# Optimization experiments

Hardware: AMD Instinct MI355X
Metric: run time of the kernel (lower is better)

Reference implementation:

```python
import jax, jax.numpy as jnp
import numpy as np

B, T, DIM, H = 32, 1024, 512, 8
HD = DIM // H
HID = int(DIM * 4.0)
EPS = 1e-6
SCALE = HD ** -0.5


def _ln(t, g, b):
    m = t.mean(-1, keepdims=True)
    var = ((t - m) ** 2).mean(-1, keepdims=True)
    return (t - m) * jax.lax.rsqrt(var + EPS) * g + b


def setup_inputs() -> dict:
    key = jax.random.key(0)
    ks = jax.random.split(key, 10)
    n = lambda k, s: jax.random.normal(k, s, dtype=jnp.float32)
    w = lambda k, s: n(k, s) * 0.02
    z = lambda d: jnp.zeros((d,), dtype=jnp.float32)
    o = lambda d: jnp.ones((d,), dtype=jnp.float32)
    return {
        'x': n(ks[0], (B, T, DIM)),
        'k': n(ks[1], (T, H, B, HD)),
        'v': n(ks[2], (T, H, B, HD)),
        'Wqkv': w(ks[3], (DIM, 3 * DIM)), 'bqkv': z(3 * DIM),
        'Wsa': w(ks[4], (DIM, DIM)), 'bsa': z(DIM),
        'Wq': w(ks[5], (DIM, DIM)), 'bq': z(DIM),
        'Wed': w(ks[6], (DIM, DIM)), 'bed': z(DIM),
        'g1': o(DIM), 'be1': z(DIM),
        'g2': o(DIM), 'be2': z(DIM),
        'g3': o(DIM), 'be3': z(DIM),
        'W1': w(ks[7], (DIM, HID)), 'b1': z(HID),
        'W2': w(ks[8], (HID, DIM)), 'b2': z(DIM),
    }


def _decoder_block(x, k, v, Wqkv, bqkv, Wsa, bsa, Wq, bq, Wed, bed,
                   g1, be1, g2, be2, g3, be3, W1, b1, W2, b2):
    # ---- self-attention (faithful to the original, degenerate einsums) ----
    qkv = x @ Wqkv + bqkv                                        # [B,T,3*DIM]
    qkv = qkv.reshape(B, T, 3, H, HD).transpose(2, 1, 3, 0, 4)   # [3,T,H,B,HD]
    q, sk, sv = qkv[0], qkv[1], qkv[2]
    dp = jnp.einsum('kabc,qdef->qabe', sk, q) * SCALE            # [T,H,B,B]
    scores = jax.nn.softmax(dp, axis=-1)
    wa = jnp.einsum('qabc,kdef->bqaf', scores, sv).reshape(B, T, DIM)
    attn = wa @ Wsa + bsa
    an1 = _ln(attn + x, g1, be1)
    # ---- encoder-decoder attention ----
    qe = (an1 @ Wq + bq).reshape(B, T, H, HD).transpose(1, 2, 0, 3)  # [T,H,B,HD]
    dp2 = jnp.einsum('abkd,abqd->abqk', k, qe) * SCALE           # [T,H,B,B]
    sc2 = jax.nn.softmax(dp2, axis=-1)
    wa2 = jnp.einsum('abts,abse->tabe', sc2, v).reshape(B, T, DIM)
    attn2 = wa2 @ Wed + bed
    an2 = _ln(attn2 + x, g2, be2)
    # ---- MLP (exact GELU, as nn.GELU default) ----
    hmid = jax.nn.gelu(an2 @ W1 + b1, approximate=False)
    z = hmid @ W2 + b2
    return _ln(z + an2, g3, be3)


def reference(x, k, v, Wqkv, bqkv, Wsa, bsa, Wq, bq, Wed, bed,
              g1, be1, g2, be2, g3, be3, W1, b1, W2, b2):
    return _decoder_block(x, k, v, Wqkv, bqkv, Wsa, bsa, Wq, bq, Wed, bed,
                          g1, be1, g2, be2, g3, be3, W1, b1, W2, b2)
```

## Files before the change

kernel.cpp:

```cpp
#include <hip/hip_runtime.h>
#include <hip/hip_bf16.h>
#include <math.h>

#define Bn 32
#define Tn 1024
#define DIMn 512
#define Hn 8
#define HDn 64
#define HIDn 2048
#define Mn 32768

using short8 = __attribute__((ext_vector_type(8))) short;
using half8  = __attribute__((ext_vector_type(8))) _Float16;
using f32x4  = __attribute__((ext_vector_type(4))) float;
typedef unsigned short u16;
typedef unsigned int   u32;

__device__ __forceinline__ u16 f2h(float x) {
  _Float16 h = (_Float16)x;
  return __builtin_bit_cast(u16, h);
}
__device__ __forceinline__ float h2f(u16 u) {
  return (float)__builtin_bit_cast(_Float16, u);
}
__device__ __forceinline__ u32 pack2h(float a, float b) {
  return (u32)f2h(a) | ((u32)f2h(b) << 16);
}
__device__ __forceinline__ void gld16(const void* g, void* l) {
  __builtin_amdgcn_global_load_lds((const __attribute__((address_space(1))) u32*)g,
                                   (__attribute__((address_space(3))) u32*)l, 16, 0, 0);
}
__device__ __forceinline__ float wredsum(float v) {
  #pragma unroll
  for (int d = 1; d < 64; d <<= 1) v += __shfl_xor(v, d, 64);
  return v;
}
__device__ __forceinline__ void barrier_mem() {
  asm volatile("" ::: "memory");
  __builtin_amdgcn_s_barrier();
  asm volatile("" ::: "memory");
}
__device__ __forceinline__ float fast_gelu(float v) {
  const float ax = fabsf(v) * 0.70710678118654752f;
  const float t = 1.0f / (1.0f + 0.3275911f * ax);
  const float p = ((((1.061405429f * t - 1.453152027f) * t) + 1.421413741f) * t - 0.284496736f) * t + 0.254829592f;
  const float y = 1.0f - p * t * __expf(-ax * ax);
  const float erfv = (v >= 0.f) ? y : -y;
  return 0.5f * v * (1.0f + erfv);
}

__global__ __launch_bounds__(256) void colsum1(const float* __restrict__ x, float* __restrict__ part) {
  const int b = blockIdx.x, t = threadIdx.x;
  const float* p = x + (size_t)b * 128 * DIMn;
  float a0 = 0.f, a1 = 0.f;
  for (int r = 0; r < 128; ++r) {
    a0 += p[r * DIMn + t];
    a1 += p[r * DIMn + t + 256];
  }
  part[b * DIMn + t] = a0;
  part[b * DIMn + t + 256] = a1;
}

__global__ __launch_bounds__(256) void colsum2(const float* __restrict__ part, float* __restrict__ xs) {
  const int c = blockIdx.x * 256 + threadIdx.x;
  float a = 0.f;
  for (int b = 0; b < 256; ++b) a += part[b * DIMn + c];
  xs[c] = a;
}

__global__ __launch_bounds__(256) void sv_k(const float* __restrict__ xs, const float* __restrict__ Wqkv,
                                            const float* __restrict__ bqkv, float* __restrict__ SVp) {
  __shared__ float xsh[512];
  __shared__ float red[4][64];
  const int h = blockIdx.x, q = threadIdx.x >> 6, f = threadIdx.x & 63;
  xsh[threadIdx.x] = xs[threadIdx.x];
  xsh[threadIdx.x + 256] = xs[threadIdx.x + 256];
  __syncthreads();
  const int colb = 2 * DIMn + h * HDn + f;
  float acc = 0.f;
  for (int i = q * 128; i < q * 128 + 128; ++i) acc += xsh[i] * Wqkv[(size_t)i * 1536 + colb];
  red[q][f] = acc;
  __syncthreads();
  if (q == 0)
    SVp[h * 64 + f] = red[0][f] + red[1][f] + red[2][f] + red[3][f] + 32768.0f * bqkv[colb];
}

__global__ __launch_bounds__(256) void attnc2_k(const float* __restrict__ SVp, const float* __restrict__ Wsa,
                                                const float* __restrict__ bsa, float* __restrict__ attnc) {
  __shared__ float SVs[64];
  __shared__ float red[4][64];
  const int q = threadIdx.x >> 6, jj = threadIdx.x & 63;
  if (threadIdx.x < 64) {
    float s = 0.f;
    #pragma unroll
    for (int h = 0; h < 8; ++h) s += SVp[h * 64 + threadIdx.x];
    SVs[threadIdx.x] = s;
  }
  __syncthreads();
  const int j = blockIdx.x * 64 + jj;
  float acc = 0.f;
  for (int i = q * 128; i < q * 128 + 128; ++i) acc += SVs[i & 63] * Wsa[(size_t)i * DIMn + j];
  red[q][jj] = acc;
  __syncthreads();
  if (q == 0) attnc[j] = red[0][jj] + red[1][jj] + red[2][jj] + red[3][jj] + bsa[j];
}

__global__ __launch_bounds__(256) void wtrans(const float* __restrict__ W, u16* __restrict__ WT, int K, int N) {
  __shared__ float tile[64][65];
  const int n0 = blockIdx.x * 64, k0 = blockIdx.y * 64;
  const int t = threadIdx.x;
  #pragma unroll
  for (int i = 0; i < 16; ++i) {
    const int fl = i * 256 + t, r = fl >> 6, c = fl & 63;
    tile[r][c] = W[(size_t)(k0 + r) * N + n0 + c];
  }
  __syncthreads();
  #pragma unroll
  for (int i = 0; i < 16; ++i) {
    const int fl = i * 256 + t, r = fl >> 6, c = fl & 63;
    WT[(size_t)(n0 + r) * K + k0 + c] = f2h(tile[c][r]);
  }
}

template <int MODE>
__global__ __launch_bounds__(256) void ln_k(const void* __restrict__ Ap, const void* __restrict__ Bp,
                                            const float* __restrict__ cv, const float* __restrict__ g,
                                            const float* __restrict__ be, void* __restrict__ outp) {
  const int row = blockIdx.x * 4 + (threadIdx.x >> 6);
  const int l = threadIdx.x & 63;
  const size_t base = (size_t)row * DIMn + l * 8;
  float v[8];
  if (MODE == 0 || MODE == 2) {
    const float* a = (const float*)Ap + base;
    float4 x0 = *(const float4*)a;
    float4 x1 = *(const float4*)(a + 4);
    v[0] = x0.x; v[1] = x0.y; v[2] = x0.z; v[3] = x0.w;
    v[4] = x1.x; v[5] = x1.y; v[6] = x1.z; v[7] = x1.w;
  } else {
    short8 s = *(const short8*)((const u16*)Ap + base);
    #pragma unroll
    for (int i = 0; i < 8; ++i) v[i] = h2f((u16)s[i]);
  }
  if (MODE == 0) {
    float4 c0 = *(const float4*)(cv + l * 8);
    float4 c1 = *(const float4*)(cv + l * 8 + 4);
    v[0] += c0.x; v[1] += c0.y; v[2] += c0.z; v[3] += c0.w;
    v[4] += c1.x; v[5] += c1.y; v[6] += c1.z; v[7] += c1.w;
  } else if (MODE == 1) {
    const float* b = (const float*)Bp + base;
    float4 x0 = *(const float4*)b;
    float4 x1 = *(const float4*)(b + 4);
    v[0] += x0.x; v[1] += x0.y; v[2] += x0.z; v[3] += x0.w;
    v[4] += x1.x; v[5] += x1.y; v[6] += x1.z; v[7] += x1.w;
  } else {
    short8 s2 = *(const short8*)((const u16*)Bp + base);
    #pragma unroll
    for (int i = 0; i < 8; ++i) v[i] += h2f((u16)s2[i]);
  }
  float s = 0.f;
  #pragma unroll
  for (int i = 0; i < 8; ++i) s += v[i];
  s = wredsum(s);
  const float mean = s * (1.0f / 512.0f);
  float q = 0.f;
  #pragma unroll
  for (int i = 0; i < 8; ++i) { const float d = v[i] - mean; q += d * d; }
  q = wredsum(q);
  const float rs = rsqrtf(q * (1.0f / 512.0f) + 1e-6f);
  float gg[8], bb[8];
  {
    float4 g0 = *(const float4*)(g + l * 8);
    float4 g1 = *(const float4*)(g + l * 8 + 4);
    float4 b0 = *(const float4*)(be + l * 8);
    float4 b1 = *(const float4*)(be + l * 8 + 4);
    gg[0] = g0.x; gg[1] = g0.y; gg[2] = g0.z; gg[3] = g0.w;
    gg[4] = g1.x; gg[5] = g1.y; gg[6] = g1.z; gg[7] = g1.w;
    bb[0] = b0.x; bb[1] = b0.y; bb[2] = b0.z; bb[3] = b0.w;
    bb[4] = b1.x; bb[5] = b1.y; bb[6] = b1.z; bb[7] = b1.w;
  }
  float y[8];
  #pragma unroll
  for (int i = 0; i < 8; ++i) y[i] = (v[i] - mean) * rs * gg[i] + bb[i];
  if (MODE == 2) {
    float* o = (float*)outp + base;
    *(float4*)o = make_float4(y[0], y[1], y[2], y[3]);
    *(float4*)(o + 4) = make_float4(y[4], y[5], y[6], y[7]);
  } else {
    short8 o;
    #pragma unroll
    for (int i = 0; i < 8; ++i) o[i] = (short)f2h(y[i]);
    *(short8*)((u16*)outp + base) = o;
  }
}

#define CPAD 140
template <bool GELU, bool OBF>
__global__ __launch_bounds__(256) void gemm_bt(const u16* __restrict__ A, const u16* __restrict__ BT,
                                               const float* __restrict__ bias, u16* __restrict__ OB,
                                               float* __restrict__ OF, int Ni, int Ki, int gridX) {
  __shared__ u16 smem[16384];
  const int tid = threadIdx.x;
  const int l = tid & 63, w = tid >> 6, wr = w >> 1, wc = w & 1;

  int wg = blockIdx.x;
  const int nwg = gridDim.x;
  if ((nwg & 7) == 0) {
    const int q = nwg >> 3;
    wg = (wg & 7) * q + (wg >> 3);
  }
  const int bx = wg % gridX, by = wg / gridX;
  const int m0 = by * 128, n0 = bx * 128;
  const int r16 = l & 15, g4 = l >> 4;

  const u16* ga = A + (size_t)(m0 + (tid >> 2)) * (size_t)Ki + (tid & 3) * 8;
  const u16* gb = BT + (size_t)(n0 + (tid >> 2)) * (size_t)Ki + (tid & 3) * 8;
  const int ldst = tid * 8;

  int aoff[4], boff[4];
  #pragma unroll
  for (int i = 0; i < 4; ++i) {
    aoff[i] = (wr * 64 + i * 16 + r16) * 32 + g4 * 8;
    boff[i] = (wc * 64 + i * 16 + r16) * 32 + g4 * 8;
  }
  f32x4 acc[4][4] = {};

  auto STAGE = [&](int kk, int cur) {
    u16* As = smem + cur * 8192;
    u16* Bs = As + 4096;
    gld16(ga + kk, &As[ldst]);
    gld16(ga + kk + (size_t)64 * Ki, &As[ldst + 2048]);
    gld16(gb + kk, &Bs[ldst]);
    gld16(gb + kk + (size_t)64 * Ki, &Bs[ldst + 2048]);
  };
  auto COMPUTE = [&](int cur) {
    const u16* As = smem + cur * 8192;
    const u16* Bs = As + 4096;
    half8 af[4], bf[4];
    #pragma unroll
    for (int i = 0; i < 4; ++i) af[i] = *(const half8*)&As[aoff[i]];
    #pragma unroll
    for (int i = 0; i < 4; ++i) bf[i] = *(const half8*)&Bs[boff[i]];
    #pragma unroll
    for (int mi = 0; mi < 4; ++mi)
      #pragma unroll
      for (int ni = 0; ni < 4; ++ni)
        acc[mi][ni] = __builtin_amdgcn_mfma_f32_16x16x32_f16(af[mi], bf[ni], acc[mi][ni], 0, 0, 0);
  };

  const int nt = Ki >> 5;
  STAGE(0, 0);
  for (int t = 0; t < nt - 1; ++t) {
    STAGE((t + 1) * 32, (t + 1) & 1);
    asm volatile("s_waitcnt vmcnt(4)" ::: "memory");
    __builtin_amdgcn_s_barrier();
    asm volatile("" ::: "memory");
    COMPUTE(t & 1);
    barrier_mem();
  }
  asm volatile("s_waitcnt vmcnt(0)" ::: "memory");
  __builtin_amdgcn_s_barrier();
  asm volatile("" ::: "memory");
  COMPUTE((nt - 1) & 1);

  if (OBF) {
    barrier_mem();
    #pragma unroll
    for (int p = 0; p < 2; ++p) {
      if (wr == p) {
        #pragma unroll
        for (int ni = 0; ni < 4; ++ni) {
          const int col = wc * 64 + ni * 16 + r16;
          const float bv = bias[n0 + col];
          #pragma unroll
          for (int mi = 0; mi < 4; ++mi) {
            #pragma unroll
            for (int r = 0; r < 4; ++r) {
              float v = acc[mi][ni][r] + bv;
              if (GELU) v = fast_gelu(v);
              smem[(mi * 16 + g4 * 4 + r) * CPAD + col] = f2h(v);
            }
          }
        }
      }
      barrier_mem();
      #pragma unroll
      for (int j = 0; j < 4; ++j) {
        const int row = (tid >> 4) + j * 16;
        const int c0 = (tid & 15) * 8;
        *(short8*)(OB + (size_t)(m0 + p * 64 + row) * Ni + n0 + c0) = *(const short8*)&smem[row * CPAD + c0];
      }
      if (p == 0) barrier_mem();
    }
  } else {
    #pragma unroll
    for (int ni = 0; ni < 4; ++ni) {
      const int col = n0 + wc * 64 + ni * 16 + r16;
      const float bv = bias[col];
      #pragma unroll
      for (int mi = 0; mi < 4; ++mi) {
        const int rowb = m0 + wr * 64 + mi * 16 + g4 * 4;
        #pragma unroll
        for (int r = 0; r < 4; ++r) {
          float v = acc[mi][ni][r] + bv;
          if (GELU) v = fast_gelu(v);
          OF[(size_t)(rowb + r) * Ni + col] = v;
        }
      }
    }
  }
}

__global__ __launch_bounds__(64) void attn_k(const u16* __restrict__ qe, const float* __restrict__ kin,
                                             const float* __restrict__ vin, u16* __restrict__ wa2) {
  const int t = blockIdx.x >> 3;
  const int h = blockIdx.x & 7;
  const int l = threadIdx.x;
  __shared__ u16 Kq[32 * 80];
  __shared__ u16 Qq[32 * 80];
  __shared__ u16 VT[64 * 48];
  __shared__ u16 Ps[32 * 48];

  const float* kp = kin + (size_t)blockIdx.x * 2048;
  const float* vp = vin + (size_t)blockIdx.x * 2048;
  #pragma unroll
  for (int i = 0; i < 8; ++i) {
    const int fl = i * 256 + l * 4;
    const int r = fl >> 6, c = fl & 63;
    float4 kv = *(const float4*)(kp + fl);
    float4 vv = *(const float4*)(vp + fl);
    *(u32*)&Kq[r * 80 + c]     = pack2h(kv.x, kv.y);
    *(u32*)&Kq[r * 80 + c + 2] = pack2h(kv.z, kv.w);
    VT[(c + 0) * 48 + r] = f2h(vv.x);
    VT[(c + 1) * 48 + r] = f2h(vv.y);
    VT[(c + 2) * 48 + r] = f2h(vv.z);
    VT[(c + 3) * 48 + r] = f2h(vv.w);
  }
  {
    const int qb = l >> 1, hf = l & 1;
    const u16* qp = qe + (size_t)(qb * Tn + t) * DIMn + h * HDn + hf * 32;
    #pragma unroll
    for (int j = 0; j < 4; ++j) {
      short8 d = *(const short8*)(qp + j * 8);
      *(short8*)&Qq[qb * 80 + hf * 32 + j * 8] = d;
    }
  }
  __syncthreads();

  const int r16 = l & 15, g4 = l >> 4;
  f32x4 sacc[2][2] = {};
  #pragma unroll
  for (int kk = 0; kk < 2; ++kk) {
    half8 aQ0 = *(const half8*)&Qq[r16 * 80 + kk * 32 + g4 * 8];
    half8 aQ1 = *(const half8*)&Qq[(16 + r16) * 80 + kk * 32 + g4 * 8];
    half8 bK0 = *(const half8*)&Kq[r16 * 80 + kk * 32 + g4 * 8];
    half8 bK1 = *(const half8*)&Kq[(16 + r16) * 80 + kk * 32 + g4 * 8];
    sacc[0][0] = __builtin_amdgcn_mfma_f32_16x16x32_f16(aQ0, bK0, sacc[0][0], 0, 0, 0);
    sacc[0][1] = __builtin_amdgcn_mfma_f32_16x16x32_f16(aQ0, bK1, sacc[0][1], 0, 0, 0);
    sacc[1][0] = __builtin_amdgcn_mfma_f32_16x16x32_f16(aQ1, bK0, sacc[1][0], 0, 0, 0);
    sacc[1][1] = __builtin_amdgcn_mfma_f32_16x16x32_f16(aQ1, bK1, sacc[1][1], 0, 0, 0);
  }
  #pragma unroll
  for (int m = 0; m < 2; ++m) {
    #pragma unroll
    for (int r = 0; r < 4; ++r) {
      const float a0 = sacc[m][0][r] * 0.125f;
      const float a1 = sacc[m][1][r] * 0.125f;
      float mx = fmaxf(a0, a1);
      #pragma unroll
      for (int d = 1; d < 16; d <<= 1) mx = fmaxf(mx, __shfl_xor(mx, d, 64));
      const float e0 = __expf(a0 - mx), e1 = __expf(a1 - mx);
      float sm = e0 + e1;
      #pragma unroll
      for (int d = 1; d < 16; d <<= 1) sm += __shfl_xor(sm, d, 64);
      const float inv = 1.0f / sm;
      const int rr = m * 16 + g4 * 4 + r;
      Ps[rr * 48 + r16]      = f2h(e0 * inv);
      Ps[rr * 48 + 16 + r16] = f2h(e1 * inv);
    }
  }
  __syncthreads();

  half8 aP0 = *(const half8*)&Ps[r16 * 48 + g4 * 8];
  half8 aP1 = *(const half8*)&Ps[(16 + r16) * 48 + g4 * 8];
  f32x4 oacc[2][4] = {};
  #pragma unroll
  for (int nn = 0; nn < 4; ++nn) {
    half8 bV = *(const half8*)&VT[(nn * 16 + r16) * 48 + g4 * 8];
    oacc[0][nn] = __builtin_amdgcn_mfma_f32_16x16x32_f16(aP0, bV, oacc[0][nn], 0, 0, 0);
    oacc[1][nn] = __builtin_amdgcn_mfma_f32_16x16x32_f16(aP1, bV, oacc[1][nn], 0, 0, 0);
  }
  #pragma unroll
  for (int m = 0; m < 2; ++m) {
    #pragma unroll
    for (int r = 0; r < 4; ++r) {
      const int qb = m * 16 + g4 * 4 + r;
      u16* op = wa2 + (size_t)(qb * Tn + t) * DIMn + h * HDn;
      #pragma unroll
      for (int nn = 0; nn < 4; ++nn)
        op[nn * 16 + r16] = f2h(oacc[m][nn][r]);
    }
  }
}

extern "C" void kernel_launch(void* const* d_in, const int* in_sizes, int n_in,
                              void* d_out, int out_size, void* d_ws, size_t ws_size,
                              hipStream_t stream) {
  (void)in_sizes; (void)n_in; (void)out_size;
  const float* x    = (const float*)d_in[0];
  const float* kin  = (const float*)d_in[1];
  const float* vin  = (const float*)d_in[2];
  const float* Wqkv = (const float*)d_in[3];
  const float* bqkv = (const float*)d_in[4];
  const float* Wsa  = (const float*)d_in[5];
  const float* bsa  = (const float*)d_in[6];
  const float* Wq   = (const float*)d_in[7];
  const float* bq   = (const float*)d_in[8];
  const float* Wed  = (const float*)d_in[9];
  const float* bed  = (const float*)d_in[10];
  const float* g1   = (const float*)d_in[11];
  const float* be1  = (const float*)d_in[12];
  const float* g2   = (const float*)d_in[13];
  const float* be2  = (const float*)d_in[14];
  const float* g3   = (const float*)d_in[15];
  const float* be3  = (const float*)d_in[16];
  const float* W1   = (const float*)d_in[17];
  const float* b1   = (const float*)d_in[18];
  const float* W2   = (const float*)d_in[19];
  const float* b2   = (const float*)d_in[20];

  char* ws = (char*)d_ws;
  float* xs    = (float*)(ws);
  float* SVp   = (float*)(ws + (2 << 10));
  float* attnc = (float*)(ws + (4 << 10));
  float* part  = (float*)(ws + (6 << 10));
  u16* wqT  = (u16*)(ws + (1 << 20));
  u16* wedT = (u16*)(ws + (1 << 20) + (512 << 10));
  u16* w1T  = (u16*)(ws + (2 << 20));
  u16* w2T  = (u16*)(ws + (4 << 20));
  u16* Abuf = (u16*)(ws + (6 << 20));
  const size_t HOFF = 38ull << 20;
  u16* hmid = (u16*)(ws + HOFF);

  u16* an1  = Abuf;
  u16* wa2  = Abuf;
  u16* an2b = Abuf;
  u16*   qe   = (u16*)d_out;
  u16*   a2bf = (u16*)d_out;
  float* zf   = (float*)d_out;

  long long avail = (long long)ws_size - (long long)HOFF;
  int crows = (avail > 0) ? (int)(avail / (HIDn * 2)) : 128;
  crows = (crows / 128) * 128;
  if (crows < 128) crows = 128;
  if (crows > Mn) crows = Mn;

  colsum1<<<256, 256, 0, stream>>>(x, part);
  colsum2<<<2, 256, 0, stream>>>(part, xs);
  sv_k<<<8, 256, 0, stream>>>(xs, Wqkv, bqkv, SVp);
  attnc2_k<<<8, 256, 0, stream>>>(SVp, Wsa, bsa, attnc);

  wtrans<<<dim3(8, 8),  256, 0, stream>>>(Wq,  wqT,  512, 512);
  wtrans<<<dim3(8, 8),  256, 0, stream>>>(Wed, wedT, 512, 512);
  wtrans<<<dim3(32, 8), 256, 0, stream>>>(W1,  w1T,  512, 2048);
  wtrans<<<dim3(8, 32), 256, 0, stream>>>(W2,  w2T,  2048, 512);

  ln_k<0><<<Mn / 4, 256, 0, stream>>>(x, nullptr, attnc, g1, be1, an1);
  gemm_bt<false, true><<<1024, 256, 0, stream>>>(an1, wqT, bq, qe, nullptr, 512, 512, 4);
  attn_k<<<Tn * Hn, 64, 0, stream>>>(qe, kin, vin, wa2);
  gemm_bt<false, true><<<1024, 256, 0, stream>>>(wa2, wedT, bed, a2bf, nullptr, 512, 512, 4);
  ln_k<1><<<Mn / 4, 256, 0, stream>>>(a2bf, x, nullptr, g2, be2, an2b);
  for (int r0 = 0; r0 < Mn; r0 += crows) {
    int rc = Mn - r0; if (rc > crows) rc = crows;
    gemm_bt<true, true><<<16 * (rc / 128), 256, 0, stream>>>(an2b + (size_t)r0 * DIMn, w1T, b1, hmid, nullptr, HIDn, DIMn, 16);
    gemm_bt<false, false><<<4 * (rc / 128), 256, 0, stream>>>(hmid, w2T, b2, nullptr, zf + (size_t)r0 * DIMn, DIMn, HIDn, 4);
  }
  ln_k<2><<<Mn / 4, 256, 0, stream>>>(zf, an2b, nullptr, g3, be3, d_out);
}
```

Measured before the change: 482.9 us.

## Replace double-buffered GEMM staging with single buffer to raise occupancy

```diff
diff --git a/kernel.cpp b/kernel.cpp
--- a/kernel.cpp
+++ b/kernel.cpp
@@ -34,11 +34,6 @@
   #pragma unroll
   for (int d = 1; d < 64; d <<= 1) v += __shfl_xor(v, d, 64);
   return v;
-}
-__device__ __forceinline__ void barrier_mem() {
-  asm volatile("" ::: "memory");
-  __builtin_amdgcn_s_barrier();
-  asm volatile("" ::: "memory");
 }
 __device__ __forceinline__ float fast_gelu(float v) {
   const float ax = fabsf(v) * 0.70710678118654752f;
@@ -193,12 +188,12 @@
   }
 }
 
-#define CPAD 140
+#define CPAD 144
 template <bool GELU, bool OBF>
-__global__ __launch_bounds__(256) void gemm_bt(const u16* __restrict__ A, const u16* __restrict__ BT,
-                                               const float* __restrict__ bias, u16* __restrict__ OB,
-                                               float* __restrict__ OF, int Ni, int Ki, int gridX) {
-  __shared__ u16 smem[16384];
+__global__ __launch_bounds__(256, 6) void gemm_bt(const u16* __restrict__ A, const u16* __restrict__ BT,
+                                                  const float* __restrict__ bias, u16* __restrict__ OB,
+                                                  float* __restrict__ OF, int Ni, int Ki, int gridX) {
+  __shared__ u16 smem[9216];
   const int tid = threadIdx.x;
   const int l = tid & 63, w = tid >> 6, wr = w >> 1, wc = w & 1;
 
@@ -220,50 +215,30 @@
   #pragma unroll
   for (int i = 0; i < 4; ++i) {
     aoff[i] = (wr * 64 + i * 16 + r16) * 32 + g4 * 8;
-    boff[i] = (wc * 64 + i * 16 + r16) * 32 + g4 * 8;
+    boff[i] = 4096 + (wc * 64 + i * 16 + r16) * 32 + g4 * 8;
   }
   f32x4 acc[4][4] = {};
 
-  auto STAGE = [&](int kk, int cur) {
-    u16* As = smem + cur * 8192;
-    u16* Bs = As + 4096;
-    gld16(ga + kk, &As[ldst]);
-    gld16(ga + kk + (size_t)64 * Ki, &As[ldst + 2048]);
-    gld16(gb + kk, &Bs[ldst]);
-    gld16(gb + kk + (size_t)64 * Ki, &Bs[ldst + 2048]);
-  };
-  auto COMPUTE = [&](int cur) {
-    const u16* As = smem + cur * 8192;
-    const u16* Bs = As + 4096;
+  for (int k0 = 0; k0 < Ki; k0 += 32) {
+    gld16(ga + k0, &smem[ldst]);
+    gld16(ga + k0 + (size_t)64 * Ki, &smem[ldst + 2048]);
+    gld16(gb + k0, &smem[4096 + ldst]);
+    gld16(gb + k0 + (size_t)64 * Ki, &smem[4096 + ldst + 2048]);
+    __syncthreads();
     half8 af[4], bf[4];
     #pragma unroll
-    for (int i = 0; i < 4; ++i) af[i] = *(const half8*)&As[aoff[i]];
-    #pragma unroll
-    for (int i = 0; i < 4; ++i) bf[i] = *(const half8*)&Bs[boff[i]];
+    for (int i = 0; i < 4; ++i) af[i] = *(const half8*)&smem[aoff[i]];
+    #pragma unroll
+    for (int i = 0; i < 4; ++i) bf[i] = *(const half8*)&smem[boff[i]];
     #pragma unroll
     for (int mi = 0; mi < 4; ++mi)
       #pragma unroll
       for (int ni = 0; ni < 4; ++ni)
         acc[mi][ni] = __builtin_amdgcn_mfma_f32_16x16x32_f16(af[mi], bf[ni], acc[mi][ni], 0, 0, 0);
-  };
-
-  const int nt = Ki >> 5;
-  STAGE(0, 0);
-  for (int t = 0; t < nt - 1; ++t) {
-    STAGE((t + 1) * 32, (t + 1) & 1);
-    asm volatile("s_waitcnt vmcnt(4)" ::: "memory");
-    __builtin_amdgcn_s_barrier();
-    asm volatile("" ::: "memory");
-    COMPUTE(t & 1);
-    barrier_mem();
-  }
-  asm volatile("s_waitcnt vmcnt(0)" ::: "memory");
-  __builtin_amdgcn_s_barrier();
-  asm volatile("" ::: "memory");
-  COMPUTE((nt - 1) & 1);
+    __syncthreads();
+  }
 
   if (OBF) {
-    barrier_mem();
     #pragma unroll
     for (int p = 0; p < 2; ++p) {
       if (wr == p) {
@@ -282,14 +257,14 @@
           }
         }
       }
-      barrier_mem();
+      __syncthreads();
       #pragma unroll
       for (int j = 0; j < 4; ++j) {
         const int row = (tid >> 4) + j * 16;
         const int c0 = (tid & 15) * 8;
         *(short8*)(OB + (size_t)(m0 + p * 64 + row) * Ni + n0 + c0) = *(const short8*)&smem[row * CPAD + c0];
       }
-      if (p == 0) barrier_mem();
+      if (p == 0) __syncthreads();
     }
   } else {
     #pragma unroll
```

New measurement: 1.480 ms. 3.06x slower.
